# Kernel tuning notes

Measured on AMD Instinct MI355X. Metric: run time of the kernel, lower is better.

## Reference

```python
import jax, jax.numpy as jnp
import numpy as np

BATCH = 512
HIDDEN_DIM = 4096
NUM_CODES = 32
CODE_DIM = 64
CODEBOOK_SIZE = 1024


def _lsa_single(cost):
    """Rectangular Hungarian (Jonker-Volgenant shortest augmenting path).
    cost: [n, m] with n <= m. Returns, for each row, the assigned column,
    minimizing total cost (matches scipy.optimize.linear_sum_assignment)."""
    n, m = cost.shape
    u = np.zeros(n + 1)
    v = np.zeros(m + 1)
    p = np.zeros(m + 1, dtype=np.int64)  # p[j]: row matched to col j (1-based); 0 = free
    for i in range(1, n + 1):
        p[0] = i
        j0 = 0
        minv = np.full(m + 1, np.inf)
        way = np.zeros(m + 1, dtype=np.int64)
        used = np.zeros(m + 1, dtype=bool)
        while True:
            used[j0] = True
            i0 = p[j0]
            free = ~used
            free[0] = False
            jfree = np.nonzero(free)[0]
            cur = cost[i0 - 1, jfree - 1] - u[i0] - v[jfree]
            upd = cur < minv[jfree]
            minv[jfree[upd]] = cur[upd]
            way[jfree[upd]] = j0
            k = jfree[np.argmin(minv[jfree])]
            delta = minv[k]
            u[p[used]] += delta
            v[used] -= delta
            minv[free] -= delta
            j0 = k
            if p[j0] == 0:
                break
        while j0 != 0:  # augment along the path
            j1 = way[j0]
            p[j0] = p[j1]
            j0 = j1
    ans = np.empty(n, dtype=np.int64)
    for j in range(1, m + 1):
        if p[j] > 0:
            ans[p[j] - 1] = j - 1
    return ans


def _lsa_batch(costs):
    costs = np.asarray(costs, dtype=np.float64)
    return np.stack([_lsa_single(c) for c in costs]).astype(np.int32)


def setup_inputs() -> dict:
    key = jax.random.key(0)
    ks = jax.random.split(key, 4)
    return {
        "x": jax.random.normal(ks[0], (BATCH, HIDDEN_DIM), jnp.float32),
        "codebook": jax.random.normal(ks[1], (CODEBOOK_SIZE, CODE_DIM), jnp.float32),
        "enc_w": jax.random.normal(ks[2], (NUM_CODES * CODE_DIM, HIDDEN_DIM), jnp.float32) * 0.02,
        "enc_b": jnp.zeros((NUM_CODES * CODE_DIM,), jnp.float32),
        "dec_w": jax.random.normal(ks[3], (HIDDEN_DIM, NUM_CODES * CODE_DIM), jnp.float32) * 0.02,
        "dec_b": jnp.zeros((HIDDEN_DIM,), jnp.float32),
    }


def reference(x, codebook, enc_w, enc_b, dec_w, dec_b):
    bs = x.shape[0]
    # encoder (torch Linear: y = x @ W.T + b)
    e = (x @ enc_w.T + enc_b).reshape(bs, NUM_CODES, CODE_DIM)
    ef = e.reshape(-1, CODE_DIM)  # [bs*num_codes, code_dim]
    # pairwise Euclidean distances to codebook entries [bs*num_codes, codebook_size]
    d2 = (jnp.sum(ef * ef, axis=1, keepdims=True)
          + jnp.sum(codebook * codebook, axis=1)
          - 2.0 * (ef @ codebook.T))
    dist = jnp.sqrt(jnp.maximum(d2, 0.0)).reshape(bs, NUM_CODES, CODEBOOK_SIZE)
    # per-sample Hungarian assignment (original uses scipy on CPU; sqrt is
    # monotone so the optimal assignment is identical)
    indices = jax.pure_callback(
        _lsa_batch,
        jax.ShapeDtypeStruct((bs, NUM_CODES), jnp.int32),
        jax.lax.stop_gradient(dist),
    )
    flat_idx = indices.reshape(-1)  # matches torch's concatenated flat indices
    q = codebook[flat_idx].reshape(bs, NUM_CODES, CODE_DIM)
    # straight-through estimator
    q_st = e + jax.lax.stop_gradient(q - e)
    r = q_st.reshape(bs, NUM_CODES * CODE_DIM) @ dec_w.T + dec_b
    return (r, q, e, flat_idx)
```

## Files before the change

### kernel.cpp

```cpp
#include <hip/hip_runtime.h>
#include <hip/hip_bf16.h>
#include <stdint.h>

#define BATCH 512
#define HID   4096
#define NC    32
#define CD    64
#define CB    1024
#define NCD   2048

typedef unsigned short u16;
typedef unsigned int   u32;
typedef __attribute__((ext_vector_type(8))) short short8;
typedef __attribute__((ext_vector_type(4))) float f32x4;

#define WAVE_SYNC()  asm volatile("s_waitcnt lgkmcnt(0)" ::: "memory")
#define SCHED_FENCE() __builtin_amdgcn_sched_barrier(0)

__device__ inline u16 bf16_rne(float f) {
  u32 u = __builtin_bit_cast(u32, f);
  u32 r = u + 0x7FFFu + ((u >> 16) & 1u);
  return (u16)(r >> 16);
}
__device__ inline float bf16_f32(u16 h) {
  u32 u = ((u32)h) << 16;
  return __builtin_bit_cast(float, u);
}
__device__ inline void split3(float a, u16& h1, u16& h2, u16& h3) {
  h1 = bf16_rne(a);
  float r1 = a - bf16_f32(h1);
  h2 = bf16_rne(r1);
  float r2 = r1 - bf16_f32(h2);
  h3 = bf16_rne(r2);
}
__device__ inline f32x4 mfma16(short8 a, short8 b, f32x4 c) {
  return __builtin_amdgcn_mfma_f32_16x16x32_bf16(a, b, c, 0, 0, 0);
}
__device__ inline void gload_lds16(const u16* g, u16* l) {
  __builtin_amdgcn_global_load_lds(
      (const __attribute__((address_space(1))) u32*)(const void*)g,
      (__attribute__((address_space(3))) u32*)(void*)l, 16, 0, 0);
}

union H8 { u16 h[8]; short8 v; };

template<int K>
__global__ __launch_bounds__(256) void conv_split3(
    const float* __restrict__ src, u16* __restrict__ d1,
    u16* __restrict__ d2, u16* __restrict__ d3) {
  __shared__ float st[4][16][36];
  const int t = threadIdx.x;
  const int wv = t >> 6, l = t & 63;
  const int g = blockIdx.x * 4 + wv;
  const int rowbase = (g / (K / 32)) * 16;
  const int kbase   = (g % (K / 32)) * 32;
  {
    const float* s = src + (size_t)(rowbase + (l >> 2)) * K + kbase + (l & 3) * 8;
    *(f32x4*)&st[wv][l >> 2][(l & 3) * 8]     = *(const f32x4*)s;
    *(f32x4*)&st[wv][l >> 2][(l & 3) * 8 + 4] = *(const f32x4*)(s + 4);
  }
  __syncthreads();
  float vv[8];
  *(f32x4*)&vv[0] = *(const f32x4*)&st[wv][l & 15][(l >> 4) * 8];
  *(f32x4*)&vv[4] = *(const f32x4*)&st[wv][l & 15][(l >> 4) * 8 + 4];
  H8 o1, o2, o3;
#pragma unroll
  for (int i = 0; i < 8; ++i) split3(vv[i], o1.h[i], o2.h[i], o3.h[i]);
  size_t off = (size_t)g * 512 + l * 8;
  *(short8*)(d1 + off) = o1.v;
  *(short8*)(d2 + off) = o2.v;
  *(short8*)(d3 + off) = o3.v;
}

template<int K>
__global__ __launch_bounds__(256) void conv_split1(
    const float* __restrict__ src, u16* __restrict__ d1) {
  __shared__ float st[4][16][36];
  const int t = threadIdx.x;
  const int wv = t >> 6, l = t & 63;
  const int g = blockIdx.x * 4 + wv;
  const int rowbase = (g / (K / 32)) * 16;
  const int kbase   = (g % (K / 32)) * 32;
  {
    const float* s = src + (size_t)(rowbase + (l >> 2)) * K + kbase + (l & 3) * 8;
    *(f32x4*)&st[wv][l >> 2][(l & 3) * 8]     = *(const f32x4*)s;
    *(f32x4*)&st[wv][l >> 2][(l & 3) * 8 + 4] = *(const f32x4*)(s + 4);
  }
  __syncthreads();
  float vv[8];
  *(f32x4*)&vv[0] = *(const f32x4*)&st[wv][l & 15][(l >> 4) * 8];
  *(f32x4*)&vv[4] = *(const f32x4*)&st[wv][l & 15][(l >> 4) * 8 + 4];
  H8 o1;
#pragma unroll
  for (int i = 0; i < 8; ++i) o1.h[i] = bf16_rne(vv[i]);
  *(short8*)(d1 + (size_t)g * 512 + l * 8) = o1.v;
}

__global__ __launch_bounds__(256, 3) void k1_gemm(
    const u16* __restrict__ A1, const u16* __restrict__ A2,
    const u16* __restrict__ A3,
    const u16* __restrict__ B1, const u16* __restrict__ B2,
    const u16* __restrict__ B3, float* __restrict__ part) {
  __shared__ u16 lds_all[48 * 512];
  const int t = threadIdx.x;
  const int wid = t >> 6, lane = t & 63;
  const int wrow = wid >> 1, wcol = wid & 1;
  const int d = blockIdx.x + (blockIdx.y << 2) + (blockIdx.z << 6);
  const int xcd = d & 7, sl = d >> 3;
  const int panel = (xcd << 3) + (sl >> 2);
  const int bm = (sl & 3) * 128;
  const int bn = (panel & 15) * 128;
  const int kz = panel >> 4;
  const int ks0 = kz * 32;

  const u16* gp[12];
#pragma unroll
  for (int i = 0; i < 12; ++i) {
    const int b = wid + 4 * i;
    const int op = b >> 3;
    const int rf = b & 7;
    const int rf0 = (op >= 3) ? (bn >> 4) : (bm >> 4);
    const u16* base = (op == 0) ? A1 : (op == 1) ? A2 : (op == 2) ? A3
                    : (op == 3) ? B1 : (op == 4) ? B2 : B3;
    gp[i] = base + (((size_t)(rf0 + rf)) * 128 + ks0) * 512 + lane * 8;
  }

  f32x4 acc[4][4];
#pragma unroll
  for (int r = 0; r < 4; ++r)
#pragma unroll
    for (int c = 0; c < 4; ++c) acc[r][c] = (f32x4)0.f;

  for (int ks = 0; ks < 32; ++ks) {
#pragma unroll
    for (int i = 0; i < 12; ++i) {
      gload_lds16(gp[i], &lds_all[(wid + 4 * i) * 512]);
      gp[i] += 512;
    }
    __syncthreads();
    short8 b0[4], b1[4], b2[4];
#pragma unroll
    for (int c = 0; c < 4; ++c) {
      const int cf = wcol * 4 + c;
      b0[c] = *(const short8*)&lds_all[(24 + 0 * 8 + cf) * 512 + lane * 8];
      b1[c] = *(const short8*)&lds_all[(24 + 1 * 8 + cf) * 512 + lane * 8];
      b2[c] = *(const short8*)&lds_all[(24 + 2 * 8 + cf) * 512 + lane * 8];
    }
#pragma unroll
    for (int r = 0; r < 4; ++r) {
      const int rf = wrow * 4 + r;
      short8 a0 = *(const short8*)&lds_all[(0 * 8 + rf) * 512 + lane * 8];
      short8 a1 = *(const short8*)&lds_all[(1 * 8 + rf) * 512 + lane * 8];
      short8 a2 = *(const short8*)&lds_all[(2 * 8 + rf) * 512 + lane * 8];
#pragma unroll
      for (int c = 0; c < 4; ++c) {
        f32x4 dd = acc[r][c];
        dd = mfma16(a0, b0[c], dd);
        dd = mfma16(a0, b1[c], dd);
        dd = mfma16(a1, b0[c], dd);
        dd = mfma16(a1, b1[c], dd);
        dd = mfma16(a0, b2[c], dd);
        dd = mfma16(a2, b0[c], dd);
        acc[r][c] = dd;
      }
    }
    __syncthreads();
  }
  float* P = part + (size_t)kz * BATCH * NCD;
#pragma unroll
  for (int r = 0; r < 4; ++r)
#pragma unroll
    for (int c = 0; c < 4; ++c) {
      int row = bm + wrow * 64 + r * 16 + (lane >> 4) * 4;
      int col = bn + wcol * 64 + c * 16 + (lane & 15);
#pragma unroll
      for (int i = 0; i < 4; ++i)
        P[(size_t)(row + i) * NCD + col] = acc[r][c][i];
    }
}

__global__ __launch_bounds__(256) void k_reduce_bias(
    const float* __restrict__ part, const float* __restrict__ bias,
    float* __restrict__ e) {
  size_t o = ((size_t)blockIdx.x * 256 + threadIdx.x) * 4;
  int n = (int)(o & (NCD - 1));
  f32x4 s = *(const f32x4*)(part + o);
  s += *(const f32x4*)(part + (size_t)1 * BATCH * NCD + o);
  s += *(const f32x4*)(part + (size_t)2 * BATCH * NCD + o);
  s += *(const f32x4*)(part + (size_t)3 * BATCH * NCD + o);
  s += *(const f32x4*)(bias + n);
  *(f32x4*)(e + o) = s;
}

__global__ __launch_bounds__(512) void k3_gemm(
    const u16* __restrict__ Ab, const u16* __restrict__ Bb,
    const float* __restrict__ bias, float* __restrict__ C) {
  __shared__ u16 As[4][64][8];
  __shared__ u16 Bs[8][64][8];
  const int t = threadIdx.x;
  const int wid = t >> 6, lane = t & 63;
  const int wrow = wid >> 2, wcol = wid & 3;
  const int d = blockIdx.x + (blockIdx.y << 3);
  const int xcd = d & 7, sl = d >> 3;
  const int bn = ((xcd << 2) + (sl >> 3)) * 128;
  const int bm = (sl & 7) * 64;
  f32x4 acc[2][2];
#pragma unroll
  for (int r = 0; r < 2; ++r)
#pragma unroll
    for (int c = 0; c < 2; ++c) acc[r][c] = (f32x4)0.f;

  for (int ks = 0; ks < 64; ++ks) {
    {
      size_t gb = (((size_t)(bn >> 4) + wid) * 64 + ks) * 512 + lane * 8;
      gload_lds16(Bb + gb, &Bs[wid][0][0]);
      if (wid < 4) {
        size_t ga = (((size_t)(bm >> 4) + wid) * 64 + ks) * 512 + lane * 8;
        gload_lds16(Ab + ga, &As[wid][0][0]);
      }
    }
    __syncthreads();
    short8 a[2], b[2];
#pragma unroll
    for (int r = 0; r < 2; ++r) a[r] = *(const short8*)&As[wrow * 2 + r][lane][0];
#pragma unroll
    for (int c = 0; c < 2; ++c) b[c] = *(const short8*)&Bs[wcol * 2 + c][lane][0];
#pragma unroll
    for (int r = 0; r < 2; ++r)
#pragma unroll
      for (int c = 0; c < 2; ++c) acc[r][c] = mfma16(a[r], b[c], acc[r][c]);
    __syncthreads();
  }
#pragma unroll
  for (int r = 0; r < 2; ++r)
#pragma unroll
    for (int c = 0; c < 2; ++c) {
      int row = bm + wrow * 32 + r * 16 + (lane >> 4) * 4;
      int col = bn + wcol * 32 + c * 16 + (lane & 15);
      float bb = bias[col];
#pragma unroll
      for (int i = 0; i < 4; ++i)
        C[(size_t)(row + i) * HID + col] = acc[r][c][i] + bb;
    }
}

__global__ __launch_bounds__(512) void k_cost(
    const float* __restrict__ e_glob,
    const float* __restrict__ codebook,
    float* __restrict__ cost) {
  __shared__ u16 Ea[2][3][8][64][8];
  __shared__ u16 Cbs[2][3][8][64][8];
  __shared__ float enorm[128], cnorm[128];
  const int t = threadIdx.x;
  const int wid = t >> 6, lane = t & 63;
  const int wrow = wid >> 2, wcol = wid & 3;
  const int r0 = blockIdx.x * 128;
  const int c0 = blockIdx.y * 128;

  {
    const int fr = lane & 15, kc = lane >> 4;
    const float* ea = e_glob   + (size_t)(r0 + wid * 16 + fr) * CD + kc * 8;
    const float* cb = codebook + (size_t)(c0 + wid * 16 + fr) * CD + kc * 8;
#pragma unroll
    for (int ks = 0; ks < 2; ++ks) {
      float va[8], vb[8];
      *(f32x4*)&va[0] = *(const f32x4*)(ea + ks * 32);
      *(f32x4*)&va[4] = *(const f32x4*)(ea + ks * 32 + 4);
      *(f32x4*)&vb[0] = *(const f32x4*)(cb + ks * 32);
      *(f32x4*)&vb[4] = *(const f32x4*)(cb + ks * 32 + 4);
      H8 a1, a2, a3, b1, b2, b3;
#pragma unroll
      for (int i = 0; i < 8; ++i) {
        split3(va[i], a1.h[i], a2.h[i], a3.h[i]);
        split3(vb[i], b1.h[i], b2.h[i], b3.h[i]);
      }
      *(short8*)&Ea[ks][0][wid][lane][0] = a1.v;
      *(short8*)&Ea[ks][1][wid][lane][0] = a2.v;
      *(short8*)&Ea[ks][2][wid][lane][0] = a3.v;
      *(short8*)&Cbs[ks][0][wid][lane][0] = b1.v;
      *(short8*)&Cbs[ks][1][wid][lane][0] = b2.v;
      *(short8*)&Cbs[ks][2][wid][lane][0] = b3.v;
    }
  }
  if (t < 256) {
    const int which = t >> 7, idx = t & 127;
    const float* p = which ? codebook + (size_t)(c0 + idx) * CD
                           : e_glob   + (size_t)(r0 + idx) * CD;
    float s = 0.f;
#pragma unroll
    for (int k = 0; k < 16; ++k) {
      f32x4 v = *(const f32x4*)(p + k * 4);
      s += v.x * v.x + v.y * v.y + v.z * v.z + v.w * v.w;
    }
    if (which) cnorm[idx] = s; else enorm[idx] = s;
  }
  __syncthreads();

  f32x4 acc[4][2];
#pragma unroll
  for (int r = 0; r < 4; ++r)
#pragma unroll
    for (int c = 0; c < 2; ++c) acc[r][c] = (f32x4)0.f;
#pragma unroll
  for (int ks = 0; ks < 2; ++ks) {
    short8 a0[4], a1[4], a2[4], b0[2], b1[2], b2[2];
#pragma unroll
    for (int r = 0; r < 4; ++r) {
      a0[r] = *(const short8*)&Ea[ks][0][wrow * 4 + r][lane][0];
      a1[r] = *(const short8*)&Ea[ks][1][wrow * 4 + r][lane][0];
      a2[r] = *(const short8*)&Ea[ks][2][wrow * 4 + r][lane][0];
    }
#pragma unroll
    for (int c = 0; c < 2; ++c) {
      b0[c] = *(const short8*)&Cbs[ks][0][wcol * 2 + c][lane][0];
      b1[c] = *(const short8*)&Cbs[ks][1][wcol * 2 + c][lane][0];
      b2[c] = *(const short8*)&Cbs[ks][2][wcol * 2 + c][lane][0];
    }
#pragma unroll
    for (int r = 0; r < 4; ++r)
#pragma unroll
      for (int c = 0; c < 2; ++c) {
        f32x4 dd = acc[r][c];
        dd = mfma16(a0[r], b0[c], dd);
        dd = mfma16(a0[r], b1[c], dd);
        dd = mfma16(a1[r], b0[c], dd);
        dd = mfma16(a1[r], b1[c], dd);
        dd = mfma16(a0[r], b2[c], dd);
        dd = mfma16(a2[r], b0[c], dd);
        acc[r][c] = dd;
      }
  }
#pragma unroll
  for (int r = 0; r < 4; ++r)
#pragma unroll
    for (int c = 0; c < 2; ++c) {
      const int rl = wrow * 64 + r * 16 + (lane >> 4) * 4;
      const int cl = wcol * 32 + c * 16 + (lane & 15);
      const float cn = cnorm[cl];
#pragma unroll
      for (int i = 0; i < 4; ++i) {
        float d2 = enorm[rl + i] + cn - 2.f * acc[r][c][i];
        cost[(size_t)(r0 + rl + i) * CB + c0 + cl] = sqrtf(fmaxf(d2, 0.f));
      }
    }
}

__global__ __launch_bounds__(64, 1) void k_assign(
    const float* __restrict__ cost_g, const float* __restrict__ codebook,
    float* __restrict__ q_out, float* __restrict__ idx_out) {
  __shared__ int idxl[32];
  const int lane = threadIdx.x;
  const int s = blockIdx.x;
  const float* __restrict__ cost = cost_g + (size_t)s * NC * CB;

  double v_[16], minv_[16];
  u32 wp_[16];
  double u_val = 0.0;
#pragma unroll
  for (int r = 0; r < 16; ++r) { v_[r] = 0.0; wp_[r] = 0; }

  float pf[16];
#pragma unroll
  for (int r = 0; r < 16; ++r) pf[r] = cost[r * 64 + lane];

  for (int i = 1; i <= NC; ++i) {
#pragma unroll
    for (int r = 0; r < 16; ++r) minv_[r] = 1e300;
    u32 col_used = 0;
    unsigned long long rowmask = 0ull;
    int j0 = 0;
    int i0 = i;
    float cc[16];
#pragma unroll
    for (int r = 0; r < 16; ++r) cc[r] = pf[r];
    int first = 1;
    for (int guard = 0; guard < 1056; ++guard) {
      rowmask |= (1ull << i0);
      const double ui0 = __shfl(u_val, i0);
      if (first && i < NC) {
#pragma unroll
        for (int r = 0; r < 16; ++r)
          pf[r] = cost[(size_t)i * CB + r * 64 + lane];
      }
      first = 0;
      double bv = 1e301; int bj = 1 << 20;
#pragma unroll
      for (int r = 0; r < 16; ++r) {
        const int j = 1 + lane + r * 64;
        if (!((col_used >> r) & 1u)) {
          double cur = (double)cc[r] - ui0 - v_[r];
          if (cur < minv_[r]) { minv_[r] = cur; wp_[r] = (wp_[r] & 0xFFFF0000u) | (u32)j0; }
          if (minv_[r] < bv) { bv = minv_[r]; bj = j; }
        }
      }
#pragma unroll
      for (int off = 1; off < 64; off <<= 1) {
        double ov = __shfl_xor(bv, off);
        int oj = __shfl_xor(bj, off);
        if (ov < bv || (ov == bv && oj < bj)) { bv = ov; bj = oj; }
      }
      const double delta = bv;
      const int k = bj;
      const int rk = (k - 1) >> 6, kl = (k - 1) & 63;
      u32 sel = 0;
#pragma unroll
      for (int r = 0; r < 16; ++r) if (r == rk) sel = wp_[r];
      const int pmk = ((u32)__shfl((int)sel, kl)) >> 16;
      float ccn[16];
      if (pmk > 0) {
        const float* crow = cost + (size_t)(pmk - 1) * CB;
#pragma unroll
        for (int r = 0; r < 16; ++r) ccn[r] = crow[r * 64 + lane];
      }
      if ((rowmask >> lane) & 1ull) u_val += delta;
#pragma unroll
      for (int r = 0; r < 16; ++r) {
        const int j = 1 + lane + r * 64;
        if ((col_used >> r) & 1u) v_[r] -= delta;
        else {
          minv_[r] -= delta;
          if (j == k) col_used |= (1u << r);
        }
      }
      j0 = k;
      if (pmk == 0) break;
      i0 = pmk;
#pragma unroll
      for (int r = 0; r < 16; ++r) cc[r] = ccn[r];
    }
    int jj = j0;
    while (jj != 0) {
      const int rj = (jj - 1) >> 6, lj = (jj - 1) & 63;
      u32 wsel = 0;
#pragma unroll
      for (int r = 0; r < 16; ++r) if (r == rj) wsel = wp_[r];
      const int j1 = ((u32)__shfl((int)wsel, lj)) & 0xFFFFu;
      int newpm;
      if (j1 == 0) newpm = i;
      else {
        const int r1 = (j1 - 1) >> 6, l1 = (j1 - 1) & 63;
        u32 psel = 0;
#pragma unroll
        for (int r = 0; r < 16; ++r) if (r == r1) psel = wp_[r];
        newpm = ((u32)__shfl((int)psel, l1)) >> 16;
      }
#pragma unroll
      for (int r = 0; r < 16; ++r)
        if (lane == lj && r == rj) wp_[r] = (wp_[r] & 0xFFFFu) | ((u32)newpm << 16);
      jj = j1;
    }
  }

#pragma unroll
  for (int r = 0; r < 16; ++r) {
    const u32 pm = wp_[r] >> 16;
    if (pm > 0) idxl[pm - 1] = lane + r * 64;
  }
  WAVE_SYNC(); SCHED_FENCE();
  if (lane < NC) idx_out[(size_t)s * NC + lane] = (float)idxl[lane];
#pragma unroll
  for (int p = 0; p < 8; ++p) {
    int vi = p * 64 + lane;
    int r = vi >> 4, c4 = vi & 15;
    int ci = idxl[r];
    float4 qv = *(const float4*)&codebook[(size_t)ci * 64 + c4 * 4];
    *(float4*)&q_out[(size_t)s * NCD + r * 64 + c4 * 4] = qv;
  }
}

extern "C" void kernel_launch(void* const* d_in, const int* in_sizes, int n_in,
                              void* d_out, int out_size, void* d_ws, size_t ws_size,
                              hipStream_t stream) {
  (void)in_sizes; (void)n_in; (void)out_size; (void)ws_size;
  const float* x        = (const float*)d_in[0];
  const float* codebook = (const float*)d_in[1];
  const float* enc_w    = (const float*)d_in[2];
  const float* enc_b    = (const float*)d_in[3];
  const float* dec_w    = (const float*)d_in[4];
  const float* dec_b    = (const float*)d_in[5];

  float* out = (float*)d_out;
  float* r_out   = out;
  float* q_out   = out + 2097152;
  float* e_out   = out + 2097152 + 1048576;
  float* idx_out = out + 2097152 + 2097152;

  char* ws = (char*)d_ws;
  u16* B1 = (u16*)ws;
  u16* B2 = (u16*)(ws + (16u << 20));
  u16* B3 = (u16*)(ws + (32u << 20));
  float* part = (float*)(ws + (48u << 20));
  float* cost_ws = (float*)ws;
  u16* qb  = (u16*)ws;
  u16* dwb = (u16*)(ws + (2u << 20));
  u16* A1 = (u16*)r_out;
  u16* A2 = (u16*)r_out + 2097152;
  u16* A3 = (u16*)q_out;

  conv_split3<HID><<<1024, 256, 0, stream>>>(x, A1, A2, A3);
  conv_split3<HID><<<4096, 256, 0, stream>>>(enc_w, B1, B2, B3);
  k1_gemm<<<dim3(4, 16, 4), 256, 0, stream>>>(A1, A2, A3, B1, B2, B3, part);
  k_reduce_bias<<<1024, 256, 0, stream>>>(part, enc_b, e_out);
  k_cost<<<dim3(128, 8), 512, 0, stream>>>(e_out, codebook, cost_ws);
  k_assign<<<BATCH, 64, 0, stream>>>(cost_ws, codebook, q_out, idx_out);
  conv_split1<NCD><<<4096, 256, 0, stream>>>(dec_w, dwb);
  conv_split1<NCD><<<512, 256, 0, stream>>>(q_out, qb);
  k3_gemm<<<dim3(8, 32), 512, 0, stream>>>(qb, dwb, dec_b, r_out);
}
```

Baseline: 222.3 us.

## Halve encoder GEMM N-tile and double k-step per barrier

The encoder split-bf16 GEMM goes from 128x128 tiles to 128x64 tiles, which doubles the grid from 256 to 512 blocks to improve CU coverage. Each loop iteration now stages two k-slices into a larger LDS buffer, so the loop runs 16 times instead of 32 and makes half as many barrier round trips. The cost is more LDS per block, a lower occupancy hint, and more total A-operand traffic, since each A tile is now reloaded for twice as many N tiles.

```diff
diff --git a/kernel.cpp b/kernel.cpp
--- a/kernel.cpp
+++ b/kernel.cpp
@@ -96,72 +96,85 @@
   *(short8*)(d1 + (size_t)g * 512 + l * 8) = o1.v;
 }
 
-__global__ __launch_bounds__(256, 3) void k1_gemm(
+__global__ __launch_bounds__(256, 2) void k1_gemm(
     const u16* __restrict__ A1, const u16* __restrict__ A2,
     const u16* __restrict__ A3,
     const u16* __restrict__ B1, const u16* __restrict__ B2,
     const u16* __restrict__ B3, float* __restrict__ part) {
-  __shared__ u16 lds_all[48 * 512];
+  __shared__ u16 lds_all[72 * 512];
   const int t = threadIdx.x;
   const int wid = t >> 6, lane = t & 63;
   const int wrow = wid >> 1, wcol = wid & 1;
-  const int d = blockIdx.x + (blockIdx.y << 2) + (blockIdx.z << 6);
+  const int d = blockIdx.x + (blockIdx.y << 2) + (blockIdx.z << 7);
   const int xcd = d & 7, sl = d >> 3;
-  const int panel = (xcd << 3) + (sl >> 2);
+  const int panel = (xcd << 4) + (sl >> 2);
   const int bm = (sl & 3) * 128;
-  const int bn = (panel & 15) * 128;
-  const int kz = panel >> 4;
+  const int bn_t = panel & 31;
+  const int kz = panel >> 5;
   const int ks0 = kz * 32;
 
-  const u16* gp[12];
-#pragma unroll
-  for (int i = 0; i < 12; ++i) {
+  const u16* gp[9];
+#pragma unroll
+  for (int i = 0; i < 9; ++i) {
     const int b = wid + 4 * i;
-    const int op = b >> 3;
-    const int rf = b & 7;
-    const int rf0 = (op >= 3) ? (bn >> 4) : (bm >> 4);
-    const u16* base = (op == 0) ? A1 : (op == 1) ? A2 : (op == 2) ? A3
-                    : (op == 3) ? B1 : (op == 4) ? B2 : B3;
-    gp[i] = base + (((size_t)(rf0 + rf)) * 128 + ks0) * 512 + lane * 8;
-  }
-
-  f32x4 acc[4][4];
+    const u16* base;
+    size_t frag;
+    if (b < 24) {
+      const int s = b >> 3, rf = b & 7;
+      base = (s == 0) ? A1 : (s == 1) ? A2 : A3;
+      frag = (size_t)((bm >> 4) + rf);
+    } else {
+      const int bb = b - 24;
+      const int s = bb >> 2, cf = bb & 3;
+      base = (s == 0) ? B1 : (s == 1) ? B2 : B3;
+      frag = (size_t)(bn_t * 4 + cf);
+    }
+    gp[i] = base + (frag * 128 + ks0) * 512 + lane * 8;
+  }
+
+  f32x4 acc[4][2];
 #pragma unroll
   for (int r = 0; r < 4; ++r)
 #pragma unroll
-    for (int c = 0; c < 4; ++c) acc[r][c] = (f32x4)0.f;
-
-  for (int ks = 0; ks < 32; ++ks) {
-#pragma unroll
-    for (int i = 0; i < 12; ++i) {
-      gload_lds16(gp[i], &lds_all[(wid + 4 * i) * 512]);
-      gp[i] += 512;
+    for (int c = 0; c < 2; ++c) acc[r][c] = (f32x4)0.f;
+
+  for (int ks = 0; ks < 16; ++ks) {
+#pragma unroll
+    for (int i = 0; i < 9; ++i) {
+      const int b = wid + 4 * i;
+      gload_lds16(gp[i],       &lds_all[b * 512]);
+      gload_lds16(gp[i] + 512, &lds_all[(36 + b) * 512]);
+      gp[i] += 1024;
     }
     __syncthreads();
-    short8 b0[4], b1[4], b2[4];
-#pragma unroll
-    for (int c = 0; c < 4; ++c) {
-      const int cf = wcol * 4 + c;
-      b0[c] = *(const short8*)&lds_all[(24 + 0 * 8 + cf) * 512 + lane * 8];
-      b1[c] = *(const short8*)&lds_all[(24 + 1 * 8 + cf) * 512 + lane * 8];
-      b2[c] = *(const short8*)&lds_all[(24 + 2 * 8 + cf) * 512 + lane * 8];
-    }
-#pragma unroll
-    for (int r = 0; r < 4; ++r) {
-      const int rf = wrow * 4 + r;
-      short8 a0 = *(const short8*)&lds_all[(0 * 8 + rf) * 512 + lane * 8];
-      short8 a1 = *(const short8*)&lds_all[(1 * 8 + rf) * 512 + lane * 8];
-      short8 a2 = *(const short8*)&lds_all[(2 * 8 + rf) * 512 + lane * 8];
-#pragma unroll
-      for (int c = 0; c < 4; ++c) {
-        f32x4 dd = acc[r][c];
-        dd = mfma16(a0, b0[c], dd);
-        dd = mfma16(a0, b1[c], dd);
-        dd = mfma16(a1, b0[c], dd);
-        dd = mfma16(a1, b1[c], dd);
-        dd = mfma16(a0, b2[c], dd);
-        dd = mfma16(a2, b0[c], dd);
-        acc[r][c] = dd;
+#pragma unroll
+    for (int ss = 0; ss < 2; ++ss) {
+      const int o = ss * 36;
+      short8 b0[2], b1[2], b2[2];
+#pragma unroll
+      for (int c = 0; c < 2; ++c) {
+        const int cf = wcol * 2 + c;
+        b0[c] = *(const short8*)&lds_all[(o + 24 + 0 * 4 + cf) * 512 + lane * 8];
+        b1[c] = *(const short8*)&lds_all[(o + 24 + 1 * 4 + cf) * 512 + lane * 8];
+        b2[c] = *(const short8*)&lds_all[(o + 24 + 2 * 4 + cf) * 512 + lane * 8];
+      }
+#pragma unroll
+      for (int r = 0; r < 4; ++r) {
+        const int rf = wrow * 4 + r;
+        short8 a0 = *(const short8*)&lds_all[(o + 0 * 8 + rf) * 512 + lane * 8];
+        short8 a1 = *(const short8*)&lds_all[(o + 1 * 8 + rf) * 512 + lane * 8];
+        short8 a2 = *(const short8*)&lds_all[(o + 2 * 8 + rf) * 512 + lane * 8];
+#pragma unroll
+        for (int c = 0; c < 2; ++c) {
+          f32x4 dd = acc[r][c];
+          dd = mfma16(a0, b0[c], dd);
+          dd = mfma16(a0, b1[c], dd);
+          dd = mfma16(a1, b0[c], dd);
+          dd = mfma16(a1, b1[c], dd);
+          dd = mfma16(a0, b2[c], dd);
+          dd = mfma16(a2, b0[c], dd);
+          acc[r][c] = dd;
+        }
       }
     }
     __syncthreads();
@@ -170,9 +183,9 @@
 #pragma unroll
   for (int r = 0; r < 4; ++r)
 #pragma unroll
-    for (int c = 0; c < 4; ++c) {
+    for (int c = 0; c < 2; ++c) {
       int row = bm + wrow * 64 + r * 16 + (lane >> 4) * 4;
-      int col = bn + wcol * 64 + c * 16 + (lane & 15);
+      int col = bn_t * 64 + wcol * 32 + c * 16 + (lane & 15);
 #pragma unroll
       for (int i = 0; i < 4; ++i)
         P[(size_t)(row + i) * NCD + col] = acc[r][c][i];
@@ -499,7 +512,7 @@
 
   conv_split3<HID><<<1024, 256, 0, stream>>>(x, A1, A2, A3);
   conv_split3<HID><<<4096, 256, 0, stream>>>(enc_w, B1, B2, B3);
-  k1_gemm<<<dim3(4, 16, 4), 256, 0, stream>>>(A1, A2, A3, B1, B2, B3, part);
+  k1_gemm<<<dim3(4, 32, 4), 256, 0, stream>>>(A1, A2, A3, B1, B2, B3, part);
   k_reduce_bias<<<1024, 256, 0, stream>>>(part, enc_b, e_out);
   k_cost<<<dim3(128, 8), 512, 0, stream>>>(e_out, codebook, cost_ws);
   k_assign<<<BATCH, 64, 0, stream>>>(cost_ws, codebook, q_out, idx_out);
```

After: 214.4 us. 1.04x faster.
